# Kernel tuning notes

Hardware: AMD Instinct MI355X
Metric: run time of the kernel (lower is better)

## Reference

```python
import jax, jax.numpy as jnp
import numpy as np

DIM = 256
L = 16            # block_size (query rows per leaf block)
H = 8             # num_heads
D = DIM // H      # head_dim = 32
KC = L + 1        # key count: L leaf nodes + 1 block (mean) node, layout '16x17'
B = 2
N = 32768         # multiple of L -> no padding path
NB = N // L       # 2048 blocks
SCALE = D ** -0.5


def setup_inputs() -> dict:
    key = jax.random.key(0)
    ks = jax.random.split(key, 8)
    x = jax.random.normal(ks[0], (B, N, DIM), jnp.float32)
    attn_mask = jax.random.randint(ks[1], (NB, L, KC), 0, 2, dtype=jnp.int32)
    ar = jnp.arange(L)
    attn_mask = attn_mask.at[:, ar, ar].set(1)  # self always visible -> no all-masked rows
    edge_feats = jax.random.normal(ks[2], (NB, L, KC, 4), jnp.float32)
    s = DIM ** -0.5
    Wqkv = jax.random.normal(ks[3], (3 * DIM, DIM), jnp.float32) * s
    bqkv = jnp.zeros((3 * DIM,), jnp.float32)
    Wproj = jax.random.normal(ks[4], (DIM, DIM), jnp.float32) * s
    bproj = jnp.zeros((DIM,), jnp.float32)
    Wgate = jax.random.normal(ks[5], (H, 4), jnp.float32) * 0.01  # nn.init.normal_(std=0.01)
    bgate = jnp.zeros((H,), jnp.float32)
    return {"x": x, "attn_mask": attn_mask, "edge_feats": edge_feats,
            "Wqkv": Wqkv, "bqkv": bqkv, "Wproj": Wproj, "bproj": bproj,
            "Wgate": Wgate, "bgate": bgate}


def reference(x, attn_mask, edge_feats, Wqkv, bqkv, Wproj, bproj, Wgate, bgate):
    # x: [B, N, C] -> blocks [B, NB, L, C]
    x_blk = x.reshape(B, NB, L, DIM)
    block_node = x_blk.mean(axis=2, keepdims=True)           # virtual block node
    kv = jnp.concatenate([x_blk, block_node], axis=2)         # [B, NB, KC, C]

    # qkv projections (slice of the fused Linear; rows are independent so math is identical)
    q = x_blk @ Wqkv[:DIM].T + bqkv[:DIM]
    k = kv @ Wqkv[DIM:2 * DIM].T + bqkv[DIM:2 * DIM]
    v = kv @ Wqkv[2 * DIM:].T + bqkv[2 * DIM:]
    q = q.reshape(B, NB, L, H, D)
    k = k.reshape(B, NB, KC, H, D)
    v = v.reshape(B, NB, KC, H, D)

    scores = jnp.einsum('bnqhd,bnkhd->bnqkh', q, k) * SCALE   # [B, NB, L, KC, H]

    # physics bias: zero out + set channel 3 = 1 for block node column and self (diagonal)
    ar = jnp.arange(L)
    unit = jnp.array([0.0, 0.0, 0.0, 1.0], edge_feats.dtype)
    bias = edge_feats.at[:, :, L, :].set(unit)                # block-node column
    bias = bias.at[:, ar, ar, :].set(unit)                    # self bias on diagonal
    bias = jnp.broadcast_to(bias[None], (B, NB, L, KC, 4))    # expand over batch

    scores = scores + bias[..., 3:4]

    mask0 = (attn_mask[None] == 0)[..., None]                 # [1, NB, L, KC, 1]
    scores = jnp.where(mask0, -jnp.inf, scores)
    attn = jax.nn.softmax(scores, axis=3)

    gate = jnp.einsum('bnqkf,hf->bnqkh', bias, Wgate) + bgate  # edge-conditioned gate
    gate = jnp.where(mask0, 0.0, gate)

    combined = attn + gate
    out = jnp.einsum('bnqkh,bnkhd->bnqhd', combined, v).reshape(B, N, DIM)
    return out @ Wproj.T + bproj
```

## Files before the change

### kernel.cpp

```cpp
#include <hip/hip_runtime.h>
#include <cstdint>
#include <cstddef>

#define B_SZ 2
#define N_SEQ 32768
#define NB 2048
#define HD 32
#define LQ 16
#define KCNT 17
#define M_ROWS 65536
#define SCALE_F 0.17677669529663687f

typedef __attribute__((ext_vector_type(8))) short sv8;
typedef __attribute__((ext_vector_type(4))) short sv4;
typedef __attribute__((ext_vector_type(4))) float f4;

__device__ __forceinline__ short f2bf(float f) {
  unsigned u = __builtin_bit_cast(unsigned, f);
  u = (u + 0x7FFFu + ((u >> 16) & 1u)) >> 16;
  return (short)u;
}
__device__ __forceinline__ float bf2f(short s) {
  unsigned u = ((unsigned)(unsigned short)s) << 16;
  return __builtin_bit_cast(float, u);
}
__device__ __forceinline__ void gload16(const void* g, void* l) {
  __builtin_amdgcn_global_load_lds(
      (const __attribute__((address_space(1))) unsigned int*)g,
      (__attribute__((address_space(3))) unsigned int*)l, 16, 0, 0);
}
__device__ __forceinline__ f4 mfma16(sv8 a, sv8 b, f4 c) {
  return __builtin_amdgcn_mfma_f32_16x16x32_bf16(a, b, c, 0, 0, 0);
}

__global__ __launch_bounds__(256) void cast_all(
    const float* __restrict__ x, const float* __restrict__ wq,
    const float* __restrict__ wp, short* __restrict__ X1,
    short* __restrict__ W1, short* __restrict__ WP1) {
  const int i = blockIdx.x * 256 + threadIdx.x;
  const float* src;
  short* dst;
  int off;
  if (i < 4194304) { src = x; dst = X1; off = i; }
  else if (i < 4194304 + 49152) { src = wq; dst = W1; off = i - 4194304; }
  else if (i < 4194304 + 49152 + 16384) { src = wp; dst = WP1; off = i - 4194304 - 49152; }
  else return;
  float4 v = ((const float4*)src)[off];
  sv4 h = {f2bf(v.x), f2bf(v.y), f2bf(v.z), f2bf(v.w)};
  *(sv4*)&dst[(size_t)off * 4] = h;
}

__global__ __launch_bounds__(256) void gemm_bf_qkv(
    const short* __restrict__ A1, const short* __restrict__ B1,
    const float* __restrict__ bias, short* __restrict__ Qbf,
    short* __restrict__ Kbf, short* __restrict__ Vbf) {
  __shared__ __align__(16) short LB[2][2][128][32];
  const int tid = threadIdx.x;
  const int w = tid >> 6, l = tid & 63;
  const int wm = w >> 1, wn = w & 1;
  const int bid = blockIdx.x;
  const int chunkc = (6 * 512) >> 3;
  const int lbid = (bid & 7) * chunkc + (bid >> 3);
  const int nti = lbid % 6, mti = lbid / 6;
  const int m0 = mti * 128, n0 = nti * 128;
  const int lr = l >> 2, lc = (l & 3) * 8;
  const int fr = l & 15, kg = (l >> 4) * 8;
  f4 acc[4][4] = {};
#pragma unroll
  for (int i = 0; i < 2; ++i) {
    const int row = w * 32 + i * 16;
    gload16(A1 + (size_t)(m0 + row + lr) * 256 + lc, (void*)&LB[0][0][row][0]);
    gload16(B1 + (size_t)(n0 + row + lr) * 256 + lc, (void*)&LB[0][1][row][0]);
  }
  asm volatile("s_waitcnt vmcnt(0)" ::: "memory");
  __builtin_amdgcn_s_barrier();
  int cur = 0;
  for (int s = 0; s < 8; ++s) {
    if (s < 7) {
      const int sk = (s + 1) * 32;
#pragma unroll
      for (int i = 0; i < 2; ++i) {
        const int row = w * 32 + i * 16;
        gload16(A1 + (size_t)(m0 + row + lr) * 256 + sk + lc,
                (void*)&LB[cur ^ 1][0][row][0]);
        gload16(B1 + (size_t)(n0 + row + lr) * 256 + sk + lc,
                (void*)&LB[cur ^ 1][1][row][0]);
      }
    }
    if (s > 0) {
      if (s < 7) asm volatile("s_waitcnt vmcnt(4)" ::: "memory");
      else asm volatile("s_waitcnt vmcnt(0)" ::: "memory");
      __builtin_amdgcn_s_barrier();
    }
    sv8 fa[4], fb[4];
#pragma unroll
    for (int t = 0; t < 4; ++t) {
      fa[t] = *(const sv8*)&LB[cur][0][wm * 64 + t * 16 + fr][kg];
      fb[t] = *(const sv8*)&LB[cur][1][wn * 64 + t * 16 + fr][kg];
    }
#pragma unroll
    for (int mt = 0; mt < 4; ++mt)
#pragma unroll
      for (int nt2 = 0; nt2 < 4; ++nt2)
        acc[mt][nt2] = mfma16(fa[mt], fb[nt2], acc[mt][nt2]);
    asm volatile("s_waitcnt lgkmcnt(0)" ::: "memory");
    __builtin_amdgcn_s_barrier();
    cur ^= 1;
  }
  short* Lout = &LB[0][0][0][0];
  const int r0 = (l >> 4) * 4;
#pragma unroll
  for (int mt = 0; mt < 4; ++mt)
#pragma unroll
    for (int nt2 = 0; nt2 < 4; ++nt2) {
      const int n = wn * 64 + nt2 * 16 + fr;
      const float bv = bias[n0 + n];
#pragma unroll
      for (int j = 0; j < 4; ++j) {
        const int m = wm * 64 + mt * 16 + r0 + j;
        Lout[m * 128 + (n ^ ((m & 7) << 3))] = f2bf(acc[mt][nt2][j] + bv);
      }
    }
  __builtin_amdgcn_s_barrier();
  short* dst = (nti < 2) ? Qbf : ((nti < 4) ? Kbf : Vbf);
  const int nnb = (nti & 1) * 128;
  const int rrow = tid >> 4, seg = (tid & 15) * 8;
#pragma unroll
  for (int p = 0; p < 8; ++p) {
    const int row = p * 16 + rrow;
    sv8 v = *(const sv8*)&Lout[row * 128 + (seg ^ ((row & 7) << 3))];
    *(sv8*)&dst[(size_t)(m0 + row) * 256 + nnb + seg] = v;
  }
}

__global__ __launch_bounds__(256) void gemm_proj1(
    const short* __restrict__ A1, const short* __restrict__ B1,
    const float* __restrict__ bias, float* __restrict__ C) {
  __shared__ __align__(16) short Ahs[2][128][32];
  __shared__ __align__(16) short Bhs[2][128][32];
  const int tid = threadIdx.x;
  const int w = tid >> 6, l = tid & 63;
  const int wm = w >> 1, wn = w & 1;
  const int bid = blockIdx.x;
  const int chunkc = (2 * 512) >> 3;
  const int lbid = (bid & 7) * chunkc + (bid >> 3);
  const int nti = lbid % 2, mti = lbid / 2;
  const int m0 = mti * 128, n0 = nti * 128;
  const int lr = l >> 2, lc = (l & 3) * 8;
  const int fr = l & 15, kg = (l >> 4) * 8;
  f4 acc[4][4] = {};
#pragma unroll
  for (int i = 0; i < 2; ++i) {
    const int row = w * 32 + i * 16;
    gload16(A1 + (size_t)(m0 + row + lr) * 256 + lc, (void*)&Ahs[0][row][0]);
    gload16(B1 + (size_t)(n0 + row + lr) * 256 + lc, (void*)&Bhs[0][row][0]);
  }
  asm volatile("s_waitcnt vmcnt(0)" ::: "memory");
  __builtin_amdgcn_s_barrier();
  int cur = 0;
  for (int s = 0; s < 8; ++s) {
    if (s < 7) {
      const int sk = (s + 1) * 32;
#pragma unroll
      for (int i = 0; i < 2; ++i) {
        const int row = w * 32 + i * 16;
        gload16(A1 + (size_t)(m0 + row + lr) * 256 + sk + lc,
                (void*)&Ahs[cur ^ 1][row][0]);
        gload16(B1 + (size_t)(n0 + row + lr) * 256 + sk + lc,
                (void*)&Bhs[cur ^ 1][row][0]);
      }
    }
    if (s > 0) {
      if (s < 7) asm volatile("s_waitcnt vmcnt(4)" ::: "memory");
      else asm volatile("s_waitcnt vmcnt(0)" ::: "memory");
      __builtin_amdgcn_s_barrier();
    }
    sv8 fa[4], fb[4];
#pragma unroll
    for (int t = 0; t < 4; ++t) {
      fa[t] = *(const sv8*)&Ahs[cur][wm * 64 + t * 16 + fr][kg];
      fb[t] = *(const sv8*)&Bhs[cur][wn * 64 + t * 16 + fr][kg];
    }
#pragma unroll
    for (int mt = 0; mt < 4; ++mt)
#pragma unroll
      for (int nt2 = 0; nt2 < 4; ++nt2)
        acc[mt][nt2] = mfma16(fa[mt], fb[nt2], acc[mt][nt2]);
    asm volatile("s_waitcnt lgkmcnt(0)" ::: "memory");
    __builtin_amdgcn_s_barrier();
    cur ^= 1;
  }
  const int r0 = (l >> 4) * 4;
#pragma unroll
  for (int mt = 0; mt < 4; ++mt)
#pragma unroll
    for (int nt2 = 0; nt2 < 4; ++nt2) {
      const int n = n0 + wn * 64 + nt2 * 16 + fr;
      const float bv = bias[n];
      const size_t mb = (size_t)(m0 + wm * 64 + mt * 16 + r0);
#pragma unroll
      for (int j = 0; j < 4; ++j) C[(mb + j) * 256 + n] = acc[mt][nt2][j] + bv;
    }
}

__global__ __launch_bounds__(256, 7) void attn_v8(
    const short* __restrict__ Qb, const short* __restrict__ Kb,
    const short* __restrict__ Vb, const int* __restrict__ amask,
    const float* __restrict__ efeat, const float* __restrict__ Wgate,
    const float* __restrict__ bgate, short* __restrict__ AO) {
  __shared__ __align__(16) short Kl[16 * 264];
  __shared__ __align__(16) short Vl[16 * 264];
  __shared__ float4 Es[LQ * KCNT];
  __shared__ int Ms[LQ * KCNT];
  short* Ol = Kl;

  const int tid = threadIdx.x;
  const int bid = blockIdx.x;
  const int g = (bid & 7) * 512 + (bid >> 3);
  const int b = g >> 11, nb = g & (NB - 1);
  const size_t tok0 = (size_t)(b * N_SEQ + nb * LQ);
  const int w = tid >> 6, l = tid & 63;
  const int ln = l & 15, lg = l >> 4;
  const f4 fzero = {0.f, 0.f, 0.f, 0.f};

  sv8 qf[2];
#pragma unroll
  for (int hh = 0; hh < 2; ++hh) {
    const int h = w * 2 + hh;
    qf[hh] = *(const sv8*)(Qb + (tok0 + ln) * 256 + h * 32 + lg * 8);
  }

#pragma unroll
  for (int i = 0; i < 2; ++i) {
    const int f = tid + i * 256;
    const int t = f >> 5, c8 = (f & 31) * 8;
    *(sv8*)&Kl[t * 264 + c8] = *(const sv8*)(Kb + (tok0 + t) * 256 + c8);
    *(sv8*)&Vl[t * 264 + c8] = *(const sv8*)(Vb + (tok0 + t) * 256 + c8);
  }
  {
    const float4* esrc = (const float4*)(efeat + (size_t)nb * LQ * KCNT * 4);
    const int* msrc = amask + (size_t)nb * LQ * KCNT;
    Es[tid] = esrc[tid];
    Ms[tid] = msrc[tid];
    if (tid < LQ * KCNT - 256) {
      Es[256 + tid] = esrc[256 + tid];
      Ms[256 + tid] = msrc[256 + tid];
    }
  }
  __syncthreads();

  const int q = ln;
  sv8 ka0 = *(const sv8*)&Kl[ln * 264 + (w * 2 + 0) * 32 + lg * 8];
  sv8 ka1 = *(const sv8*)&Kl[ln * 264 + (w * 2 + 1) * 32 + lg * 8];
  const f4 sr0 = mfma16(ka0, qf[0], fzero);
  const f4 sr1 = mfma16(ka1, qf[1], fzero);
  __syncthreads();

#pragma unroll
  for (int hh = 0; hh < 2; ++hh) {
    const int h = w * 2 + hh;
    const f4 sr = (hh == 0) ? sr0 : sr1;

    const float wg0 = Wgate[h * 4], wg1 = Wgate[h * 4 + 1];
    const float wg2 = Wgate[h * 4 + 2], wg3 = Wgate[h * 4 + 3];
    const float bg = bgate[h];

    float rs = sr[0] + sr[1] + sr[2] + sr[3];
    rs += __shfl_xor(rs, 16);
    rs += __shfl_xor(rs, 32);

    float s_[4], gt_[4];
    int vis_[4];
#pragma unroll
    for (int j = 0; j < 4; ++j) {
      const int kc = lg * 4 + j;
      float e0, e1, e2, e3;
      if (kc == q) { e0 = e1 = e2 = 0.f; e3 = 1.f; }
      else { float4 e = Es[q * KCNT + kc]; e0 = e.x; e1 = e.y; e2 = e.z; e3 = e.w; }
      const int m = Ms[q * KCNT + kc];
      vis_[j] = m;
      s_[j] = sr[j] * SCALE_F + e3;
      gt_[j] = m ? (e0 * wg0 + e1 * wg1 + e2 * wg2 + e3 * wg3 + bg) : 0.f;
    }
    const int m16 = Ms[q * KCNT + 16];
    const float s16 = rs * 0.0625f * SCALE_F + 1.0f;

    float mx = -1e30f;
#pragma unroll
    for (int j = 0; j < 4; ++j)
      if (vis_[j]) mx = fmaxf(mx, s_[j]);
    mx = fmaxf(mx, __shfl_xor(mx, 16));
    mx = fmaxf(mx, __shfl_xor(mx, 32));
    if (m16) mx = fmaxf(mx, s16);

    float p_[4], den = 0.f;
#pragma unroll
    for (int j = 0; j < 4; ++j) {
      p_[j] = vis_[j] ? __expf(s_[j] - mx) : 0.f;
      den += p_[j];
    }
    den += __shfl_xor(den, 16);
    den += __shfl_xor(den, 32);
    const float p16 = m16 ? __expf(s16 - mx) : 0.f;
    den += p16;
    const float inv = 1.f / den;
    const float gt16 = m16 ? (wg3 + bg) : 0.f;
    const float cb16 = (p16 * inv + gt16) * 0.0625f;
    float pc[4];
#pragma unroll
    for (int j = 0; j < 4; ++j) pc[j] = p_[j] * inv + gt_[j] + cb16;

    sv8 pa;
#pragma unroll
    for (int e = 0; e < 8; ++e) {
      const int kc = lg * 8 + e;
      const int src = ((kc >> 2) << 4) | q;
      const float v0 = __shfl(pc[e & 3], src);
      pa[e] = (kc < 16) ? f2bf(v0) : (short)0;
    }

#pragma unroll
    for (int t = 0; t < 2; ++t) {
      sv8 vb;
#pragma unroll
      for (int e = 0; e < 8; ++e) {
        const int vr = (lg * 8 + e) & 15;
        vb[e] = Vl[vr * 264 + h * 32 + t * 16 + ln];
      }
      f4 oacc = mfma16(pa, vb, fzero);
#pragma unroll
      for (int j = 0; j < 4; ++j)
        Ol[(lg * 4 + j) * 264 + h * 32 + t * 16 + ln] = f2bf(oacc[j]);
    }
  }
  __syncthreads();

#pragma unroll
  for (int i = 0; i < 2; ++i) {
    const int f = tid + i * 256;
    const int t = f >> 5, c8 = (f & 31) * 8;
    *(sv8*)(AO + (tok0 + t) * 256 + c8) = *(const sv8*)&Ol[t * 264 + c8];
  }
}

extern "C" void kernel_launch(void* const* d_in, const int* in_sizes, int n_in,
                              void* d_out, int out_size, void* d_ws, size_t ws_size,
                              hipStream_t stream) {
  const float* x = (const float*)d_in[0];
  const int* amask = (const int*)d_in[1];
  const float* efeat = (const float*)d_in[2];
  const float* Wqkv = (const float*)d_in[3];
  const float* bqkv = (const float*)d_in[4];
  const float* Wproj = (const float*)d_in[5];
  const float* bproj = (const float*)d_in[6];
  const float* Wgate = (const float*)d_in[7];
  const float* bgate = (const float*)d_in[8];
  float* out = (float*)d_out;

  char* ws = (char*)d_ws;
  const size_t QB_SZ = (size_t)M_ROWS * 256 * 2;
  const size_t W1_SZ = (size_t)768 * 256 * 2;
  const size_t WP1_SZ = (size_t)256 * 256 * 2;
  if (ws_size < 5 * QB_SZ + W1_SZ + WP1_SZ) return;

  short* X1 = (short*)ws;
  short* Qbf = (short*)(ws + QB_SZ);
  short* Kbf = (short*)(ws + 2 * QB_SZ);
  short* Vbf = (short*)(ws + 3 * QB_SZ);
  short* AOh = (short*)(ws + 4 * QB_SZ);
  short* W1 = (short*)(ws + 5 * QB_SZ);
  short* WP1 = (short*)(ws + 5 * QB_SZ + W1_SZ);

  const int total_f4 = 4194304 + 49152 + 16384;
  cast_all<<<dim3((total_f4 + 255) / 256), 256, 0, stream>>>(x, Wqkv, Wproj,
                                                             X1, W1, WP1);
  gemm_bf_qkv<<<dim3(6 * 512), 256, 0, stream>>>(X1, W1, bqkv, Qbf, Kbf, Vbf);
  attn_v8<<<dim3(B_SZ * NB), 256, 0, stream>>>(Qbf, Kbf, Vbf, amask, efeat,
                                               Wgate, bgate, AOh);
  gemm_proj1<<<dim3(2 * 512), 256, 0, stream>>>(AOh, WP1, bproj, out);
}
```

Before: 122.8 us.

## Fuse fp32-to-bf16 cast of x into QKV GEMM operand loading

Drops the separate pass that converted the whole activation tensor x to bf16 in workspace. The QKV GEMM now streams fp32 x tiles into LDS with an XOR swizzle and converts them to bf16 while building the MFMA fragments. This removes one full read and write of x plus its intermediate buffer. In exchange, each GEMM tile loads twice the bytes for A, and the 6 N-tiles each re-read fp32 x, so A-side global traffic doubles and conversion work is repeated per tile.

```diff
diff --git a/kernel.cpp b/kernel.cpp
--- a/kernel.cpp
+++ b/kernel.cpp
@@ -33,28 +33,27 @@
   return __builtin_amdgcn_mfma_f32_16x16x32_bf16(a, b, c, 0, 0, 0);
 }
 
-__global__ __launch_bounds__(256) void cast_all(
-    const float* __restrict__ x, const float* __restrict__ wq,
-    const float* __restrict__ wp, short* __restrict__ X1,
+__global__ __launch_bounds__(256) void cast_w(
+    const float* __restrict__ wq, const float* __restrict__ wp,
     short* __restrict__ W1, short* __restrict__ WP1) {
   const int i = blockIdx.x * 256 + threadIdx.x;
   const float* src;
   short* dst;
   int off;
-  if (i < 4194304) { src = x; dst = X1; off = i; }
-  else if (i < 4194304 + 49152) { src = wq; dst = W1; off = i - 4194304; }
-  else if (i < 4194304 + 49152 + 16384) { src = wp; dst = WP1; off = i - 4194304 - 49152; }
+  if (i < 49152) { src = wq; dst = W1; off = i; }
+  else if (i < 49152 + 16384) { src = wp; dst = WP1; off = i - 49152; }
   else return;
   float4 v = ((const float4*)src)[off];
   sv4 h = {f2bf(v.x), f2bf(v.y), f2bf(v.z), f2bf(v.w)};
   *(sv4*)&dst[(size_t)off * 4] = h;
 }
 
-__global__ __launch_bounds__(256) void gemm_bf_qkv(
-    const short* __restrict__ A1, const short* __restrict__ B1,
+__global__ __launch_bounds__(256) void gemm_f_qkv(
+    const float* __restrict__ Xf, const short* __restrict__ B1,
     const float* __restrict__ bias, short* __restrict__ Qbf,
     short* __restrict__ Kbf, short* __restrict__ Vbf) {
-  __shared__ __align__(16) short LB[2][2][128][32];
+  __shared__ __align__(16) float Af[2][128][32];
+  __shared__ __align__(16) short Bs[2][128][32];
   const int tid = threadIdx.x;
   const int w = tid >> 6, l = tid & 63;
   const int wm = w >> 1, wn = w & 1;
@@ -66,37 +65,48 @@
   const int lr = l >> 2, lc = (l & 3) * 8;
   const int fr = l & 15, kg = (l >> 4) * 8;
   f4 acc[4][4] = {};
-#pragma unroll
-  for (int i = 0; i < 2; ++i) {
-    const int row = w * 32 + i * 16;
-    gload16(A1 + (size_t)(m0 + row + lr) * 256 + lc, (void*)&LB[0][0][row][0]);
-    gload16(B1 + (size_t)(n0 + row + lr) * 256 + lc, (void*)&LB[0][1][row][0]);
-  }
+
+#define STAGE_CHUNK(buf, skf)                                                  \
+  {                                                                            \
+    _Pragma("unroll") for (int i = 0; i < 4; ++i) {                            \
+      const int row = w * 32 + i * 8 + (l >> 3);                               \
+      const int ug = (l & 7) ^ (row & 7);                                      \
+      gload16(Xf + (size_t)(m0 + row) * 256 + (skf) + ug * 4,                  \
+              (void*)&Af[buf][w * 32 + i * 8][0]);                             \
+    }                                                                          \
+    _Pragma("unroll") for (int i = 0; i < 2; ++i) {                            \
+      const int row = w * 32 + i * 16;                                         \
+      gload16(B1 + (size_t)(n0 + row + lr) * 256 + (skf) + lc,                 \
+              (void*)&Bs[buf][row][0]);                                        \
+    }                                                                          \
+  }
+
+  STAGE_CHUNK(0, 0)
   asm volatile("s_waitcnt vmcnt(0)" ::: "memory");
   __builtin_amdgcn_s_barrier();
   int cur = 0;
   for (int s = 0; s < 8; ++s) {
-    if (s < 7) {
-      const int sk = (s + 1) * 32;
-#pragma unroll
-      for (int i = 0; i < 2; ++i) {
-        const int row = w * 32 + i * 16;
-        gload16(A1 + (size_t)(m0 + row + lr) * 256 + sk + lc,
-                (void*)&LB[cur ^ 1][0][row][0]);
-        gload16(B1 + (size_t)(n0 + row + lr) * 256 + sk + lc,
-                (void*)&LB[cur ^ 1][1][row][0]);
-      }
-    }
+    if (s < 7) STAGE_CHUNK(cur ^ 1, (s + 1) * 32)
     if (s > 0) {
-      if (s < 7) asm volatile("s_waitcnt vmcnt(4)" ::: "memory");
+      if (s < 7) asm volatile("s_waitcnt vmcnt(6)" ::: "memory");
       else asm volatile("s_waitcnt vmcnt(0)" ::: "memory");
       __builtin_amdgcn_s_barrier();
     }
     sv8 fa[4], fb[4];
 #pragma unroll
     for (int t = 0; t < 4; ++t) {
-      fa[t] = *(const sv8*)&LB[cur][0][wm * 64 + t * 16 + fr][kg];
-      fb[t] = *(const sv8*)&LB[cur][1][wn * 64 + t * 16 + fr][kg];
+      const int r = wm * 64 + t * 16 + fr;
+      const int rb = r & 7;
+      const int u0 = ((l >> 4) * 2) ^ rb;
+      f4 x0 = *(const f4*)&Af[cur][r][u0 * 4];
+      f4 x1 = *(const f4*)&Af[cur][r][(u0 ^ 1) * 4];
+      sv8 o;
+      o[0] = f2bf(x0[0]); o[1] = f2bf(x0[1]);
+      o[2] = f2bf(x0[2]); o[3] = f2bf(x0[3]);
+      o[4] = f2bf(x1[0]); o[5] = f2bf(x1[1]);
+      o[6] = f2bf(x1[2]); o[7] = f2bf(x1[3]);
+      fa[t] = o;
+      fb[t] = *(const sv8*)&Bs[cur][wn * 64 + t * 16 + fr][kg];
     }
 #pragma unroll
     for (int mt = 0; mt < 4; ++mt)
@@ -107,7 +117,8 @@
     __builtin_amdgcn_s_barrier();
     cur ^= 1;
   }
-  short* Lout = &LB[0][0][0][0];
+#undef STAGE_CHUNK
+  short* Lout = (short*)&Af[0][0][0];
   const int r0 = (l >> 4) * 4;
 #pragma unroll
   for (int mt = 0; mt < 4; ++mt)
@@ -361,20 +372,18 @@
   const size_t QB_SZ = (size_t)M_ROWS * 256 * 2;
   const size_t W1_SZ = (size_t)768 * 256 * 2;
   const size_t WP1_SZ = (size_t)256 * 256 * 2;
-  if (ws_size < 5 * QB_SZ + W1_SZ + WP1_SZ) return;
-
-  short* X1 = (short*)ws;
-  short* Qbf = (short*)(ws + QB_SZ);
-  short* Kbf = (short*)(ws + 2 * QB_SZ);
-  short* Vbf = (short*)(ws + 3 * QB_SZ);
-  short* AOh = (short*)(ws + 4 * QB_SZ);
-  short* W1 = (short*)(ws + 5 * QB_SZ);
-  short* WP1 = (short*)(ws + 5 * QB_SZ + W1_SZ);
-
-  const int total_f4 = 4194304 + 49152 + 16384;
-  cast_all<<<dim3((total_f4 + 255) / 256), 256, 0, stream>>>(x, Wqkv, Wproj,
-                                                             X1, W1, WP1);
-  gemm_bf_qkv<<<dim3(6 * 512), 256, 0, stream>>>(X1, W1, bqkv, Qbf, Kbf, Vbf);
+  if (ws_size < 4 * QB_SZ + W1_SZ + WP1_SZ) return;
+
+  short* Qbf = (short*)ws;
+  short* Kbf = (short*)(ws + QB_SZ);
+  short* Vbf = (short*)(ws + 2 * QB_SZ);
+  short* AOh = (short*)(ws + 3 * QB_SZ);
+  short* W1 = (short*)(ws + 4 * QB_SZ);
+  short* WP1 = (short*)(ws + 4 * QB_SZ + W1_SZ);
+
+  cast_w<<<dim3((49152 + 16384 + 255) / 256), 256, 0, stream>>>(Wqkv, Wproj,
+                                                                W1, WP1);
+  gemm_f_qkv<<<dim3(6 * 512), 256, 0, stream>>>(x, W1, bqkv, Qbf, Kbf, Vbf);
   attn_v8<<<dim3(B_SZ * NB), 256, 0, stream>>>(Qbf, Kbf, Vbf, amask, efeat,
                                                Wgate, bgate, AOh);
   gemm_proj1<<<dim3(2 * 512), 256, 0, stream>>>(AOh, WP1, bproj, out);
```

Result: slower. 132.7 us (+8.1%).
